# Optimization experiments

Hardware: AMD Instinct MI355X
Metric: run time of the kernel (lower is better)

## Reference

```python
import jax, jax.numpy as jnp
import numpy as np

G, N, K, H, D = 16, 256, 128, 32, 768
NUM_ATOM_TYPES = 128
NUM_EDGE_TYPES = NUM_ATOM_TYPES * NUM_ATOM_TYPES  # 16384
T_STEPS = 1000


def setup_inputs() -> dict:
    key = jax.random.key(0)
    ks = jax.random.split(key, 12)
    return {
        "pos": jax.random.normal(ks[0], (G, N, 3), dtype=jnp.float32) * 3.0,
        "x": jax.random.randint(ks[1], (G, N, 1), 0, NUM_ATOM_TYPES, dtype=jnp.int32),
        "t": jax.random.randint(ks[2], (G,), 0, T_STEPS, dtype=jnp.int32),
        "means": jax.random.uniform(ks[3], (T_STEPS, K), jnp.float32, 0.0, 3.0),
        "stds": jax.random.uniform(ks[4], (T_STEPS, K), jnp.float32, 0.0, 3.0),
        "mul_w": jnp.ones((NUM_EDGE_TYPES, 1), jnp.float32),
        "bias_w": jnp.zeros((NUM_EDGE_TYPES, 1), jnp.float32),
        "w1": jax.random.normal(ks[5], (K, K), jnp.float32) / np.sqrt(K),
        "b1": jnp.zeros((K,), jnp.float32),
        "w2": jax.random.normal(ks[6], (K, H), jnp.float32) / np.sqrt(K),
        "b2": jnp.zeros((H,), jnp.float32),
        "we": jax.random.normal(ks[7], (K, D), jnp.float32) / np.sqrt(K),
        "be": jnp.zeros((D,), jnp.float32),
    }


def _forward(pos, x, t, means, stds, mul_w, bias_w, w1, b1, w2, b2, we, be):
    atoms = x[:, :, 0]  # [G, N]
    edge_types = atoms[:, :, None] * NUM_ATOM_TYPES + atoms[:, None, :]  # [G,N,N]
    pad = atoms == 0  # [G, N]
    pos = jnp.where(pad[..., None], 0.0, pos)
    # delta_pos[g,i,j] = pos[g,j] - pos[g,i]
    delta_pos = pos[:, None, :, :] - pos[:, :, None, :]  # [G,N,N,3]
    sq = jnp.sum(delta_pos * delta_pos, axis=-1)  # [G,N,N]
    dist = jnp.sqrt(jnp.where(sq > 0, sq, 1.0)) * (sq > 0)  # safe norm, grad-safe at 0
    delta_pos = delta_pos / (dist[..., None] + 1e-5)
    # Gaussian basis expansion
    mul = mul_w[edge_types]   # [G,N,N,1]
    bias = bias_w[edge_types]  # [G,N,N,1]
    xg = mul * dist[..., None] + bias  # [G,N,N,1] -> broadcasts to K
    mean = means[t][:, None, None, :]               # [G,1,1,K]
    std = jnp.abs(stds[t])[:, None, None, :] + 1e-5  # [G,1,1,K]
    a = (2.0 * 3.14159) ** 0.5
    z = (xg - mean) / std
    edge_feature = jnp.exp(-0.5 * z * z) / (a * std)  # [G,N,N,K]
    # NonLinear MLP -> attn bias per head
    h = jax.nn.gelu(edge_feature @ w1 + b1, approximate=False)
    attn_bias = h @ w2 + b2  # [G,N,N,H]
    attn_bias = jnp.transpose(attn_bias, (0, 3, 1, 2))  # [G,H,N,N]
    attn_bias = jnp.where(pad[:, None, None, :], -jnp.inf, attn_bias)
    # masked sum over source nodes + edge projection
    ef = jnp.where(pad[:, None, :, None], 0.0, edge_feature)
    sum_ef = jnp.sum(ef, axis=-2)  # [G,N,K]
    merge = sum_ef @ we + be  # [G,N,D]
    return dist, delta_pos, attn_bias, merge


def reference(pos, x, t, means, stds, mul_w, bias_w, w1, b1, w2, b2, we, be):
    return _forward(pos, x, t, means, stds, mul_w, bias_w, w1, b1, w2, b2, we, be)
```

## Files before the change

### kernel.cpp

```cpp
#include <hip/hip_runtime.h>
#include <hip/hip_bf16.h>
#include <math.h>

#define Gn 16
#define Nn 256
#define Kf 128
#define Hh 32
#define Dd 768
#define NEG_BIG (-3.0e38f)
#define INV_A 0.3989422804014327f
#define NHALF_LOG2E (-0.7213475204444817f)
#define GELU_C (-2.4554669f)

typedef __attribute__((ext_vector_type(8))) short bf16x8;
typedef __attribute__((ext_vector_type(4))) float f32x4;

static __device__ __forceinline__ float fast_exp2(float x) {
#if __has_builtin(__builtin_amdgcn_exp2f)
    return __builtin_amdgcn_exp2f(x);
#else
    return exp2f(x);
#endif
}
static __device__ __forceinline__ float fast_rcp(float x) {
#if __has_builtin(__builtin_amdgcn_rcpf)
    return __builtin_amdgcn_rcpf(x);
#else
    return 1.0f / x;
#endif
}

static __device__ __forceinline__ unsigned short f2bf(float f) {
    union { float f; unsigned int u; } v; v.f = f;
    unsigned int r = v.u + 0x7FFF + ((v.u >> 16) & 1);
    return (unsigned short)(r >> 16);
}

static __device__ __forceinline__ void load_lds16(const void* g, void* l) {
    __builtin_amdgcn_global_load_lds(
        (const __attribute__((address_space(1))) unsigned int*)g,
        (__attribute__((address_space(3))) unsigned int*)l, 16, 0, 0);
}

static __device__ __forceinline__ void stage8k(const char* gsrc, char* lbase,
                                               int wq, int lane) {
    const char* g0 = gsrc + wq * 1024 + lane * 16;
    char* l0 = lbase + wq * 1024 + lane * 16;
    load_lds16(g0, l0);
    load_lds16(g0 + 4096, l0 + 4096);
}

__global__ __launch_bounds__(256)
void prep_kernel(const float* __restrict__ w1, const float* __restrict__ w2,
                 const int* __restrict__ tarr, const float* __restrict__ means,
                 const float* __restrict__ stds,
                 char* __restrict__ w1c, char* __restrict__ w2s,
                 float4* __restrict__ coef)
{
    const int idx = blockIdx.x * 256 + threadIdx.x;
    if (idx < 2048) {
        const int ks = idx >> 9;
        const int n  = (idx >> 2) & 127;
        const int s  = idx & 3;
        unsigned short v[8];
#pragma unroll
        for (int e = 0; e < 8; ++e) {
            const int k = ks * 32 + s * 8 + e;
            v[e] = f2bf(w1[k * Kf + n]);
        }
        *(uint4*)(w1c + ks * 8192 + n * 64 + ((s ^ ((n >> 1) & 3)) << 4)) =
            *(const uint4*)v;
    } else if (idx < 2560) {
        const int e2 = idx - 2048;
        const int m = e2 >> 4, s2 = e2 & 15;
        unsigned short v[8];
#pragma unroll
        for (int e = 0; e < 8; ++e) {
            const int k = s2 * 8 + e;
            v[e] = f2bf(w2[k * Hh + m]);
        }
        *(uint4*)(w2s + m * 256 + ((s2 ^ (m & 7)) << 4)) = *(const uint4*)v;
    } else if (idx < 4608) {
        const int e3 = idx - 2560;
        const int g = e3 >> 7, k = e3 & 127;
        const int tg = tarr[g];
        const float mean = means[tg * Kf + k];
        const float sd   = fabsf(stds[tg * Kf + k]) + 1e-5f;
        const float inv  = 1.0f / sd;
        coef[g * Kf + k] =
            make_float4(mean, NHALF_LOG2E * inv * inv, log2f(inv * INV_A), 0.f);
    }
}

__global__ __launch_bounds__(256, 4)
void graph3d_attn_kernel(const float* __restrict__ pos,
                         const int* __restrict__ atoms,
                         const float* __restrict__ mul_w,
                         const float* __restrict__ bias_w,
                         const float* __restrict__ b1,
                         const float* __restrict__ b2,
                         const char* __restrict__ w1c,
                         const char* __restrict__ w2s,
                         const float4* __restrict__ coef,
                         float* __restrict__ ws_sum,
                         float* __restrict__ out_dist,
                         float* __restrict__ out_delta,
                         float* __restrict__ out_attn)
{
    const int tid  = threadIdx.x;
    const int half = blockIdx.x;
    const int i    = blockIdx.y;
    const int g    = blockIdx.z;
    const int j0   = half * 128;

    __shared__ __align__(16) unsigned short s_tile[128 * 128];
    __shared__ __align__(16) unsigned short s_chunk[4096];

    const int lane = tid & 63, wq = tid >> 6;
    const int l15 = lane & 15, lhi = lane >> 4;

    const int ai = atoms[g * Nn + i];
    float pix = pos[(g * Nn + i) * 3 + 0];
    float piy = pos[(g * Nn + i) * 3 + 1];
    float piz = pos[(g * Nn + i) * 3 + 2];
    if (ai == 0) { pix = 0.f; piy = 0.f; piz = 0.f; }

    const int jA = lane, jB = lane + 64;
    const int aA = atoms[g * Nn + j0 + jA];
    const int aB = atoms[g * Nn + j0 + jB];
    float pax = pos[(g * Nn + j0 + jA) * 3 + 0];
    float pay = pos[(g * Nn + j0 + jA) * 3 + 1];
    float paz = pos[(g * Nn + j0 + jA) * 3 + 2];
    if (aA == 0) { pax = 0.f; pay = 0.f; paz = 0.f; }
    float pbx = pos[(g * Nn + j0 + jB) * 3 + 0];
    float pby = pos[(g * Nn + j0 + jB) * 3 + 1];
    float pbz = pos[(g * Nn + j0 + jB) * 3 + 2];
    if (aB == 0) { pbx = 0.f; pby = 0.f; pbz = 0.f; }

    const float dxA = pax - pix, dyA = pay - piy, dzA = paz - piz;
    const float sqA = dxA * dxA + dyA * dyA + dzA * dzA;
    const float dA  = (sqA > 0.f) ? sqrtf(sqA) : 0.f;
    const float ivA = 1.f / (dA + 1e-5f);
    const int  etA  = ai * 128 + aA;
    const float xgA = fmaf(mul_w[etA], dA, bias_w[etA]);

    const float dxB = pbx - pix, dyB = pby - piy, dzB = pbz - piz;
    const float sqB = dxB * dxB + dyB * dyB + dzB * dzB;
    const float dB  = (sqB > 0.f) ? sqrtf(sqB) : 0.f;
    const float ivB = 1.f / (dB + 1e-5f);
    const int  etB  = ai * 128 + aB;
    const float xgB = fmaf(mul_w[etB], dB, bias_w[etB]);

    const unsigned long long mA = __ballot(aA != 0);
    const unsigned long long mB = __ballot(aB != 0);

    if (wq == (lane >> 5)) {
        const size_t base = (size_t)(g * Nn + i) * Nn + j0 + jA;
        out_dist[base] = dA;
        out_delta[base * 3 + 0] = dxA * ivA;
        out_delta[base * 3 + 1] = dyA * ivA;
        out_delta[base * 3 + 2] = dzA * ivA;
    } else if (wq == 2 + (lane >> 5)) {
        const size_t base = (size_t)(g * Nn + i) * Nn + j0 + jB;
        out_dist[base] = dB;
        out_delta[base * 3 + 0] = dxB * ivB;
        out_delta[base * 3 + 1] = dyB * ivB;
        out_delta[base * 3 + 2] = dzB * ivB;
    }

    stage8k(w1c, (char*)s_chunk, wq, lane);

    {
        const int kpl = lane >> 2, jsub = lane & 3;
        const int kp  = wq * 16 + kpl;
        const float4 c0 = coef[g * Kf + 2 * kp];
        const float4 c1 = coef[g * Kf + 2 * kp + 1];
        const float xsrc = (jsub & 2) ? xgB : xgA;
        const unsigned long long msel = (jsub & 2) ? mB : mA;
        const unsigned int mm = (jsub & 1) ? (unsigned int)(msel >> 32)
                                           : (unsigned int)msel;
        const int sbase = (jsub & 1) * 32;
        char* rowb = (char*)s_tile + jsub * 32 * 256;
        unsigned int wa[8];
#pragma unroll
        for (int s = 0; s < 8; ++s) wa[s] = (unsigned int)(4 * kp) ^ (unsigned int)(s << 4);

        float ps0 = 0.f, ps1 = 0.f;
#pragma unroll
        for (int jj = 0; jj < 32; ++jj) {
            const float xgj = __shfl(xsrc, sbase + jj);
            const float kf  = (float)((mm >> jj) & 1u);
            const float d0 = xgj - c0.x;
            const float d1 = xgj - c1.x;
            const float e0 = fast_exp2(fmaf(c0.y, d0 * d0, c0.z));
            const float e1 = fast_exp2(fmaf(c1.y, d1 * d1, c1.z));
            ps0 = fmaf(e0, kf, ps0);
            ps1 = fmaf(e1, kf, ps1);
            const __hip_bfloat162 p = __float22bfloat162_rn(make_float2(e0, e1));
            *(unsigned int*)(rowb + jj * 256 + wa[jj & 7]) = *(const unsigned int*)&p;
        }
        ps0 += __shfl_xor(ps0, 1); ps0 += __shfl_xor(ps0, 2);
        ps1 += __shfl_xor(ps1, 1); ps1 += __shfl_xor(ps1, 2);
        if (jsub == 0)
            *(float2*)&ws_sum[((size_t)(g * Nn + i) * 2 + half) * Kf + 2 * kp] =
                make_float2(ps0, ps1);
    }
    __syncthreads();

    const int jrow0 = wq * 32 + l15, jrow1 = jrow0 + 16;
    const char* tb0 = (const char*)s_tile + jrow0 * 256;
    const char* tb1 = (const char*)s_tile + jrow1 * 256;
    const int sw0 = (jrow0 & 7) << 4, sw1 = (jrow1 & 7) << 4;
    const int aoff = l15 * 64 + ((lhi ^ ((l15 >> 1) & 3)) << 4);

    f32x4 acc[8][2];
#pragma unroll
    for (int a = 0; a < 8; ++a)
#pragma unroll
        for (int b = 0; b < 2; ++b) acc[a][b] = (f32x4){0.f, 0.f, 0.f, 0.f};

#pragma unroll
    for (int ks = 0; ks < 4; ++ks) {
        if (ks) __syncthreads();
        const int kb = ks * 64 + lhi * 16;
        const bf16x8 b0  = *(const bf16x8*)(tb0 + (kb ^ sw0));
        const bf16x8 b1f = *(const bf16x8*)(tb1 + (kb ^ sw1));
        bf16x8 a[8];
#pragma unroll
        for (int nf = 0; nf < 8; ++nf)
            a[nf] = *(const bf16x8*)((const char*)s_chunk + nf * 1024 + aoff);
        __syncthreads();
        if (ks < 3) stage8k(w1c + (ks + 1) * 8192, (char*)s_chunk, wq, lane);
        else        stage8k(w2s, (char*)s_chunk, wq, lane);
#pragma unroll
        for (int nf = 0; nf < 8; ++nf) {
            acc[nf][0] = __builtin_amdgcn_mfma_f32_16x16x32_bf16(a[nf], b0,  acc[nf][0], 0, 0, 0);
            acc[nf][1] = __builtin_amdgcn_mfma_f32_16x16x32_bf16(a[nf], b1f, acc[nf][1], 0, 0, 0);
        }
    }

#pragma unroll
    for (int nf = 0; nf < 8; ++nf) {
        const float4 bb = *(const float4*)(b1 + nf * 16 + lhi * 4);
        const int colb = 32 * nf + 8 * lhi;
#pragma unroll
        for (int jf = 0; jf < 2; ++jf) {
            const char* tb = jf ? tb1 : tb0;
            const int sw = jf ? sw1 : sw0;
            float h[4];
#pragma unroll
            for (int r = 0; r < 4; ++r) {
                const float v = acc[nf][jf][r] + ((const float*)&bb)[r];
                const float sg = fast_rcp(1.0f + fast_exp2(GELU_C * v));
                h[r] = v * sg;
            }
            const __hip_bfloat162 p0 = __float22bfloat162_rn(make_float2(h[0], h[1]));
            const __hip_bfloat162 p1 = __float22bfloat162_rn(make_float2(h[2], h[3]));
            uint2 u;
            u.x = *(const unsigned int*)&p0;
            u.y = *(const unsigned int*)&p1;
            *(uint2*)(const_cast<char*>(tb) + (colb ^ sw)) = u;
        }
    }
    __syncthreads();

    f32x4 acc2[2][2];
#pragma unroll
    for (int a = 0; a < 2; ++a)
#pragma unroll
        for (int b = 0; b < 2; ++b) acc2[a][b] = (f32x4){0.f, 0.f, 0.f, 0.f};

#pragma unroll
    for (int ks = 0; ks < 4; ++ks) {
        const int kb = ks * 64 + lhi * 16;
        const bf16x8 bh0 = *(const bf16x8*)(tb0 + (kb ^ sw0));
        const bf16x8 bh1 = *(const bf16x8*)(tb1 + (kb ^ sw1));
#pragma unroll
        for (int mf = 0; mf < 2; ++mf) {
            const int m = mf * 16 + l15;
            const bf16x8 a2 = *(const bf16x8*)((const char*)s_chunk + m * 256 + (kb ^ ((m & 7) << 4)));
            acc2[mf][0] = __builtin_amdgcn_mfma_f32_16x16x32_bf16(a2, bh0, acc2[mf][0], 0, 0, 0);
            acc2[mf][1] = __builtin_amdgcn_mfma_f32_16x16x32_bf16(a2, bh1, acc2[mf][1], 0, 0, 0);
        }
    }

    const size_t attn_g = (size_t)g * Hh * (Nn * Nn) + (size_t)i * Nn + j0;
    const unsigned long long mOwn = (wq & 2) ? mB : mA;
#pragma unroll
    for (int jf = 0; jf < 2; ++jf) {
        const int jloc = wq * 32 + jf * 16 + l15;
        const int bit  = (wq & 1) * 32 + jf * 16 + l15;
        const bool keep = (mOwn >> bit) & 1ull;
#pragma unroll
        for (int mf = 0; mf < 2; ++mf) {
            const float4 b2v = *(const float4*)(b2 + mf * 16 + lhi * 4);
#pragma unroll
            for (int r = 0; r < 4; ++r) {
                const int m = mf * 16 + lhi * 4 + r;
                float v = acc2[mf][jf][r] + ((const float*)&b2v)[r];
                if (!keep) v = NEG_BIG;
                out_attn[attn_g + (size_t)m * (Nn * Nn) + jloc] = v;
            }
        }
    }
}

__global__ __launch_bounds__(256)
void graph3d_merge_kernel(const float* __restrict__ ws_sum,
                          const float* __restrict__ we,
                          const float* __restrict__ be,
                          float* __restrict__ out_merge)
{
    const int tid = threadIdx.x;
    const int bd  = blockIdx.x;
    const int r0  = blockIdx.y * 16;
    __shared__ __align__(16) float s_rows[16][128];

#pragma unroll
    for (int p = 0; p < 8; ++p) {
        const int e = p * 256 + tid;
        const int r = e >> 7, k = e & 127;
        const size_t gi = (size_t)(r0 + r);
        s_rows[r][k] = ws_sum[(gi * 2 + 0) * Kf + k] + ws_sum[(gi * 2 + 1) * Kf + k];
    }
    __syncthreads();

    const int col = bd * 256 + tid;
    float acc[16];
#pragma unroll
    for (int r = 0; r < 16; ++r) acc[r] = 0.f;

    for (int k4 = 0; k4 < 32; ++k4) {
        const int k = k4 * 4;
        const float w0 = we[(k + 0) * Dd + col];
        const float w1v = we[(k + 1) * Dd + col];
        const float w2v = we[(k + 2) * Dd + col];
        const float w3 = we[(k + 3) * Dd + col];
#pragma unroll
        for (int r = 0; r < 16; ++r) {
            const float4 s = ((const float4*)&s_rows[r][0])[k4];
            acc[r] = fmaf(s.x, w0, acc[r]);
            acc[r] = fmaf(s.y, w1v, acc[r]);
            acc[r] = fmaf(s.z, w2v, acc[r]);
            acc[r] = fmaf(s.w, w3, acc[r]);
        }
    }

    const float b = be[col];
#pragma unroll
    for (int r = 0; r < 16; ++r)
        out_merge[(size_t)(r0 + r) * Dd + col] = acc[r] + b;
}

extern "C" void kernel_launch(void* const* d_in, const int* in_sizes, int n_in,
                              void* d_out, int out_size, void* d_ws, size_t ws_size,
                              hipStream_t stream) {
    const float* pos    = (const float*)d_in[0];
    const int*   x      = (const int*)  d_in[1];
    const int*   t      = (const int*)  d_in[2];
    const float* means  = (const float*)d_in[3];
    const float* stds   = (const float*)d_in[4];
    const float* mul_w  = (const float*)d_in[5];
    const float* bias_w = (const float*)d_in[6];
    const float* w1     = (const float*)d_in[7];
    const float* b1     = (const float*)d_in[8];
    const float* w2     = (const float*)d_in[9];
    const float* b2     = (const float*)d_in[10];
    const float* we     = (const float*)d_in[11];
    const float* be     = (const float*)d_in[12];

    float* out = (float*)d_out;
    float* out_dist  = out;
    float* out_delta = out + (size_t)Gn * Nn * Nn;
    float* out_attn  = out + (size_t)Gn * Nn * Nn * 4;
    float* out_merge = out + (size_t)Gn * Nn * Nn * 4 + (size_t)Gn * Hh * Nn * Nn;

    float* ws_sum = (float*)d_ws;
    char*  w1c  = (char*)d_ws + (size_t)Gn * Nn * 2 * Kf * 4;
    char*  w2s  = w1c + 4 * 8192;
    float4* coef = (float4*)(w2s + 8192);

    prep_kernel<<<18, 256, 0, stream>>>(w1, w2, t, means, stds, w1c, w2s, coef);

    dim3 gridA(2, Nn, Gn);
    graph3d_attn_kernel<<<gridA, 256, 0, stream>>>(
        pos, x, mul_w, bias_w, b1, b2, w1c, w2s, coef,
        ws_sum, out_dist, out_delta, out_attn);

    dim3 gridB(3, 256);
    graph3d_merge_kernel<<<gridB, 256, 0, stream>>>(
        ws_sum, we, be, out_merge);
}
```

Baseline: 131.7 us.

## Remap Gaussian-basis work per lane, change W1 swizzle, split MFMA loads

Each lane now owns one k-pair and each wave owns a 32-row j block of the edge-feature tile. Previously each lane handled a k-pair for a quarter of the rows and shuffled partial sums. The per-k row sums are reduced across waves through shared memory after the MLP instead of by warp shuffles, and the W1 chunk swizzle changes to n&3. The first GEMM's A-fragment loads are split into two halves so half the MFMAs can issue before the barrier and restage. This targets the shuffle cost, LDS bank conflicts and load/MFMA overlap, at the price of two extra barriers and reuse of the tile buffer for the reduction.

```diff
diff --git a/kernel.cpp b/kernel.cpp
--- a/kernel.cpp
+++ b/kernel.cpp
@@ -68,7 +68,7 @@
             const int k = ks * 32 + s * 8 + e;
             v[e] = f2bf(w1[k * Kf + n]);
         }
-        *(uint4*)(w1c + ks * 8192 + n * 64 + ((s ^ ((n >> 1) & 3)) << 4)) =
+        *(uint4*)(w1c + ks * 8192 + n * 64 + ((s ^ (n & 3)) << 4)) =
             *(const uint4*)v;
     } else if (idx < 2560) {
         const int e2 = idx - 2048;
@@ -170,23 +170,19 @@
 
     stage8k(w1c, (char*)s_chunk, wq, lane);
 
+    float ps0 = 0.f, ps1 = 0.f;
     {
-        const int kpl = lane >> 2, jsub = lane & 3;
-        const int kp  = wq * 16 + kpl;
-        const float4 c0 = coef[g * Kf + 2 * kp];
-        const float4 c1 = coef[g * Kf + 2 * kp + 1];
-        const float xsrc = (jsub & 2) ? xgB : xgA;
-        const unsigned long long msel = (jsub & 2) ? mB : mA;
-        const unsigned int mm = (jsub & 1) ? (unsigned int)(msel >> 32)
-                                           : (unsigned int)msel;
-        const int sbase = (jsub & 1) * 32;
-        char* rowb = (char*)s_tile + jsub * 32 * 256;
-        unsigned int wa[8];
-#pragma unroll
-        for (int s = 0; s < 8; ++s) wa[s] = (unsigned int)(4 * kp) ^ (unsigned int)(s << 4);
-
-        float ps0 = 0.f, ps1 = 0.f;
-#pragma unroll
+        const int k2 = lane;
+        const float4 c0 = coef[g * Kf + 2 * k2];
+        const float4 c1 = coef[g * Kf + 2 * k2 + 1];
+        const float xsrc = (wq & 2) ? xgB : xgA;
+        const unsigned long long msel = (wq & 2) ? mB : mA;
+        const unsigned int mm = (wq & 1) ? (unsigned int)(msel >> 32)
+                                         : (unsigned int)msel;
+        const int sbase = (wq & 1) * 32;
+        char* rowbase = (char*)s_tile + wq * 32 * 256;
+        const int colb = 4 * k2;
+#pragma unroll 8
         for (int jj = 0; jj < 32; ++jj) {
             const float xgj = __shfl(xsrc, sbase + jj);
             const float kf  = (float)((mm >> jj) & 1u);
@@ -197,13 +193,9 @@
             ps0 = fmaf(e0, kf, ps0);
             ps1 = fmaf(e1, kf, ps1);
             const __hip_bfloat162 p = __float22bfloat162_rn(make_float2(e0, e1));
-            *(unsigned int*)(rowb + jj * 256 + wa[jj & 7]) = *(const unsigned int*)&p;
-        }
-        ps0 += __shfl_xor(ps0, 1); ps0 += __shfl_xor(ps0, 2);
-        ps1 += __shfl_xor(ps1, 1); ps1 += __shfl_xor(ps1, 2);
-        if (jsub == 0)
-            *(float2*)&ws_sum[((size_t)(g * Nn + i) * 2 + half) * Kf + 2 * kp] =
-                make_float2(ps0, ps1);
+            *(unsigned int*)(rowbase + jj * 256 + (colb ^ ((jj & 7) << 4))) =
+                *(const unsigned int*)&p;
+        }
     }
     __syncthreads();
 
@@ -211,7 +203,7 @@
     const char* tb0 = (const char*)s_tile + jrow0 * 256;
     const char* tb1 = (const char*)s_tile + jrow1 * 256;
     const int sw0 = (jrow0 & 7) << 4, sw1 = (jrow1 & 7) << 4;
-    const int aoff = l15 * 64 + ((lhi ^ ((l15 >> 1) & 3)) << 4);
+    const int aoff = l15 * 64 + ((lhi ^ (l15 & 3)) << 4);
 
     f32x4 acc[8][2];
 #pragma unroll
@@ -225,17 +217,26 @@
         const int kb = ks * 64 + lhi * 16;
         const bf16x8 b0  = *(const bf16x8*)(tb0 + (kb ^ sw0));
         const bf16x8 b1f = *(const bf16x8*)(tb1 + (kb ^ sw1));
-        bf16x8 a[8];
-#pragma unroll
-        for (int nf = 0; nf < 8; ++nf)
-            a[nf] = *(const bf16x8*)((const char*)s_chunk + nf * 1024 + aoff);
+        bf16x8 a0[4];
+#pragma unroll
+        for (int nf = 0; nf < 4; ++nf)
+            a0[nf] = *(const bf16x8*)((const char*)s_chunk + nf * 1024 + aoff);
+#pragma unroll
+        for (int nf = 0; nf < 4; ++nf) {
+            acc[nf][0] = __builtin_amdgcn_mfma_f32_16x16x32_bf16(a0[nf], b0,  acc[nf][0], 0, 0, 0);
+            acc[nf][1] = __builtin_amdgcn_mfma_f32_16x16x32_bf16(a0[nf], b1f, acc[nf][1], 0, 0, 0);
+        }
+        bf16x8 a1[4];
+#pragma unroll
+        for (int nf = 0; nf < 4; ++nf)
+            a1[nf] = *(const bf16x8*)((const char*)s_chunk + (nf + 4) * 1024 + aoff);
         __syncthreads();
         if (ks < 3) stage8k(w1c + (ks + 1) * 8192, (char*)s_chunk, wq, lane);
         else        stage8k(w2s, (char*)s_chunk, wq, lane);
 #pragma unroll
-        for (int nf = 0; nf < 8; ++nf) {
-            acc[nf][0] = __builtin_amdgcn_mfma_f32_16x16x32_bf16(a[nf], b0,  acc[nf][0], 0, 0, 0);
-            acc[nf][1] = __builtin_amdgcn_mfma_f32_16x16x32_bf16(a[nf], b1f, acc[nf][1], 0, 0, 0);
+        for (int nf = 0; nf < 4; ++nf) {
+            acc[nf + 4][0] = __builtin_amdgcn_mfma_f32_16x16x32_bf16(a1[nf], b0,  acc[nf + 4][0], 0, 0, 0);
+            acc[nf + 4][1] = __builtin_amdgcn_mfma_f32_16x16x32_bf16(a1[nf], b1f, acc[nf + 4][1], 0, 0, 0);
         }
     }
 
@@ -284,6 +285,18 @@
         }
     }
 
+    __syncthreads();
+    {
+        float* pt = (float*)s_tile;
+        *(float2*)&pt[wq * 128 + 2 * lane] = make_float2(ps0, ps1);
+    }
+    __syncthreads();
+    if (tid < 128) {
+        float* pt = (float*)s_tile;
+        const float s = (pt[tid] + pt[128 + tid]) + (pt[256 + tid] + pt[384 + tid]);
+        ws_sum[((size_t)(g * Nn + i) * 2 + half) * Kf + tid] = s;
+    }
+
     const size_t attn_g = (size_t)g * Hh * (Nn * Nn) + (size_t)i * Nn + j0;
     const unsigned long long mOwn = (wq & 2) ? mB : mA;
 #pragma unroll
@@ -332,10 +345,10 @@
 
     for (int k4 = 0; k4 < 32; ++k4) {
         const int k = k4 * 4;
-        const float w0 = we[(k + 0) * Dd + col];
+        const float w0  = we[(k + 0) * Dd + col];
         const float w1v = we[(k + 1) * Dd + col];
         const float w2v = we[(k + 2) * Dd + col];
-        const float w3 = we[(k + 3) * Dd + col];
+        const float w3  = we[(k + 3) * Dd + col];
 #pragma unroll
         for (int r = 0; r < 16; ++r) {
             const float4 s = ((const float4*)&s_rows[r][0])[k4];
```

Measured after the change: 129.2 us. Within noise of the previous version (-1.9%).
